# Optimization experiments

Measured on AMD Instinct MI355X. Metric: run time of the kernel, lower is better.

Reference implementation:

```python
import jax, jax.numpy as jnp
import numpy as np

NUM_HEADS = 16
THETA = 10000.0


def _rope(x, pos, theta):
    # x: [B, H, S, D], pos: [S] ints. Interleaved-pair RoPE.
    D = x.shape[-1]
    half = D // 2
    inv_freq = theta ** (-(jnp.arange(half, dtype=jnp.float32) * 2.0) / D)  # [half]
    ang = pos.astype(jnp.float32)[:, None] * inv_freq[None, :]              # [S, half]
    cos, sin = jnp.cos(ang), jnp.sin(ang)
    x1 = x[..., 0::2]
    x2 = x[..., 1::2]
    r1 = x1 * cos - x2 * sin
    r2 = x1 * sin + x2 * cos
    return jnp.stack([r1, r2], axis=-1).reshape(x.shape)


def setup_inputs() -> dict:
    key = jax.random.key(0)
    ks = jax.random.split(key, 5)
    B, S, D = 4, 2048, 1024
    scale = 1.0 / np.sqrt(D)
    x = jax.random.normal(ks[0], (B, S, D), dtype=jnp.float32)
    Wq = jax.random.normal(ks[1], (D, D), dtype=jnp.float32) * scale
    Wk = jax.random.normal(ks[2], (D, D), dtype=jnp.float32) * scale
    Wv = jax.random.normal(ks[3], (D, D), dtype=jnp.float32) * scale
    Wo = jax.random.normal(ks[4], (D, D), dtype=jnp.float32) * scale
    token_positions = jnp.arange(S, dtype=jnp.int64)
    return {"x": x, "Wq": Wq, "Wk": Wk, "Wv": Wv, "Wo": Wo,
            "token_positions": token_positions}


def reference(x, Wq, Wk, Wv, Wo, token_positions):
    B, S, D = x.shape
    H = NUM_HEADS
    hd = D // H
    # Projections (weights stored as [d_model, d_k], matching the transposed params)
    q = jnp.einsum('bsd,de->bse', x, Wq).reshape(B, S, H, hd).transpose(0, 2, 1, 3)
    k = jnp.einsum('bsd,de->bse', x, Wk).reshape(B, S, H, hd).transpose(0, 2, 1, 3)
    v = jnp.einsum('bsd,de->bse', x, Wv).reshape(B, S, H, hd).transpose(0, 2, 1, 3)
    # RoPE on q and k
    q = _rope(q, token_positions, THETA)
    k = _rope(k, token_positions, THETA)
    # Causal scaled dot-product attention
    scores = jnp.einsum('bhqd,bhkd->bhqk', q, k) / jnp.sqrt(jnp.float32(hd))
    causal = jnp.tril(jnp.ones((S, S), dtype=bool))
    scores = jnp.where(causal, scores, jnp.float32(-jnp.inf))
    attn = jax.nn.softmax(scores, axis=-1)
    o = jnp.einsum('bhqk,bhkd->bhqd', attn, v)          # [B, H, S, hd]
    o = o.transpose(0, 2, 1, 3).reshape(B, S, D)         # [B, S, D]
    return jnp.einsum('bsd,de->bse', o, Wo)
```

## Files before the change

### kernel.cpp

```cpp
#include <hip/hip_runtime.h>
#include <math.h>

#define B_ 4
#define S_ 2048
#define D_ 1024
#define H_ 16
#define HD_ 64
#define ES_F 0.180336880111f
#define KF (-0.41524101186f)

typedef unsigned short ushort_t;
typedef __attribute__((ext_vector_type(8))) short short8;
typedef __attribute__((ext_vector_type(4))) short short4_t;
typedef __attribute__((ext_vector_type(4))) float f32x4;
typedef __attribute__((ext_vector_type(16))) float f32x16;
typedef __attribute__((ext_vector_type(2))) unsigned uint2v;

typedef const void __attribute__((address_space(1))) gvoid;
typedef void __attribute__((address_space(3))) lvoid;

__device__ __forceinline__ ushort_t f2bf(float f) {
    union { float f; unsigned u; } v; v.f = f;
    unsigned r = (v.u + 0x7FFFu + ((v.u >> 16) & 1u)) >> 16;
    return (ushort_t)r;
}
__device__ __forceinline__ float fexp2(float x) {
#if __has_builtin(__builtin_amdgcn_exp2f)
    return __builtin_amdgcn_exp2f(x);
#else
    return exp2f(x);
#endif
}
__device__ __forceinline__ unsigned pk2t(float a, float b) {
    union { float f; unsigned u; } A, Bv; A.f = a; Bv.f = b;
#if __has_builtin(__builtin_amdgcn_perm)
    return __builtin_amdgcn_perm(Bv.u, A.u, 0x07060302u);
#else
    return (A.u >> 16) | (Bv.u & 0xFFFF0000u);
#endif
}
__device__ __forceinline__ short8 mk_frag(unsigned a, unsigned b, unsigned c, unsigned d) {
    union { unsigned u[4]; short8 s; } t;
    t.u[0] = a; t.u[1] = b; t.u[2] = c; t.u[3] = d; return t.s;
}

__global__ __launch_bounds__(256)
void cvt_x(const float* __restrict__ x, ushort_t* __restrict__ xb)
{
    const size_t i = ((size_t)blockIdx.x * 256 + threadIdx.x) * 8;
    float4 a = *(const float4*)&x[i];
    float4 b = *(const float4*)&x[i + 4];
    short8 o;
    o[0] = (short)f2bf(a.x); o[1] = (short)f2bf(a.y);
    o[2] = (short)f2bf(a.z); o[3] = (short)f2bf(a.w);
    o[4] = (short)f2bf(b.x); o[5] = (short)f2bf(b.y);
    o[6] = (short)f2bf(b.z); o[7] = (short)f2bf(b.w);
    *(short8*)&xb[i] = o;
}

__global__ __launch_bounds__(256)
void cvt_wt4(const float* __restrict__ W0, const float* __restrict__ W1,
             const float* __restrict__ W2, const float* __restrict__ W3,
             ushort_t* __restrict__ T0, ushort_t* __restrict__ T1,
             ushort_t* __restrict__ T2, ushort_t* __restrict__ T3)
{
    const int z = blockIdx.z;
    const float* W = (z == 0) ? W0 : (z == 1) ? W1 : (z == 2) ? W2 : W3;
    ushort_t* Wt = (z == 0) ? T0 : (z == 1) ? T1 : (z == 2) ? T2 : T3;

    __shared__ __align__(16) float T[64 * 68];
    const int t = threadIdx.x;
    const int k0 = blockIdx.y * 64, n0 = blockIdx.x * 64;
    const int row = t >> 2, c0 = (t & 3) * 16;
#pragma unroll
    for (int u = 0; u < 4; ++u)
        *(float4*)&T[row * 68 + c0 + u * 4] =
            *(const float4*)&W[(size_t)(k0 + row) * D_ + n0 + c0 + u * 4];
    __syncthreads();
    const int n = t >> 2, kc = (t & 3) * 16;
    short8 o0, o1;
#pragma unroll
    for (int kk = 0; kk < 8; ++kk) o0[kk] = (short)f2bf(T[(kc + kk) * 68 + n]);
#pragma unroll
    for (int kk = 0; kk < 8; ++kk) o1[kk] = (short)f2bf(T[(kc + 8 + kk) * 68 + n]);
    *(short8*)&Wt[(size_t)(n0 + n) * D_ + k0 + kc] = o0;
    *(short8*)&Wt[(size_t)(n0 + n) * D_ + k0 + kc + 8] = o1;
}


#define STAGE(tt, Ad, Bd) {                                                    \
    const int kk_ = (tt) * 64;                                                 \
    _Pragma("unroll") for (int i_ = 0; i_ < 4; ++i_) {                         \
        const int rb_ = (i_ * 4 + w) * 8;                                      \
        __builtin_amdgcn_global_load_lds(                                      \
            (gvoid*)&pA[(size_t)(aBase + rb_ + srow) * D_ + kk_ + sch],        \
            (lvoid*)&(Ad)[rb_ * 64], 16, 0, 0);                                \
        __builtin_amdgcn_global_load_lds(                                      \
            (gvoid*)&pB[(size_t)(bBase + rb_ + srow) * D_ + kk_ + sch],        \
            (lvoid*)&(Bd)[rb_ * 64], 16, 0, 0);                                \
    } }

#define COMPUTE(Ab, Bb) {                                                      \
    _Pragma("unroll") for (int ks = 0; ks < 4; ++ks) {                         \
        const int xr_ = (((ks * 2 + hl) ^ (lq & 7)) << 3);                     \
        short8 af0 = *(const short8*)&(Ab)[(wr * 64 + lq) * 64 + xr_];         \
        short8 af1 = *(const short8*)&(Ab)[(wr * 64 + 32 + lq) * 64 + xr_];    \
        short8 bf0 = *(const short8*)&(Bb)[(wc * 64 + lq) * 64 + xr_];         \
        short8 bf1 = *(const short8*)&(Bb)[(wc * 64 + 32 + lq) * 64 + xr_];    \
        acc[0][0] = __builtin_amdgcn_mfma_f32_32x32x16_bf16(af0, bf0, acc[0][0], 0, 0, 0); \
        acc[0][1] = __builtin_amdgcn_mfma_f32_32x32x16_bf16(af0, bf1, acc[0][1], 0, 0, 0); \
        acc[1][0] = __builtin_amdgcn_mfma_f32_32x32x16_bf16(af1, bf0, acc[1][0], 0, 0, 0); \
        acc[1][1] = __builtin_amdgcn_mfma_f32_32x32x16_bf16(af1, bf1, acc[1][1], 0, 0, 0); \
    } }

__global__ __launch_bounds__(256, 2)
void gemm_bt(const ushort_t* __restrict__ A,
             const ushort_t* __restrict__ W0, const ushort_t* __restrict__ W1,
             const ushort_t* __restrict__ W2,
             void* __restrict__ d0, void* __restrict__ d1, void* __restrict__ d2,
             const int mode_base)
{
    __shared__ __align__(16) ushort_t As[2 * 128 * 64];
    __shared__ __align__(16) ushort_t Bs[2 * 128 * 64];

    const int tid = threadIdx.x;
    const int lane = tid & 63;
    const int hl = lane >> 5;
    const int lq = lane & 31;
    const int w = tid >> 6, wr = w >> 1, wc = w & 1;
    const int z = blockIdx.z;
    const ushort_t* Wt = (z == 0) ? W0 : (z == 1) ? W1 : W2;
    const int mode = mode_base + z;
    const bool sw = (mode != 2);

    const int tokT = blockIdx.x * 128, featT = blockIdx.y * 128;
    const ushort_t* pA = sw ? Wt : A;
    const ushort_t* pB = sw ? A : Wt;
    const int aBase = sw ? featT : tokT;
    const int bBase = sw ? tokT : featT;

    const f32x16 zv16 = {0,0,0,0,0,0,0,0,0,0,0,0,0,0,0,0};
    f32x16 acc[2][2];
    acc[0][0] = zv16; acc[0][1] = zv16; acc[1][0] = zv16; acc[1][1] = zv16;

    const int srow = lane >> 3;
    const int spc  = lane & 7;
    const int sch  = (spc ^ srow) * 8;

    ushort_t* A0 = As;  ushort_t* A1 = As + 128 * 64;
    ushort_t* B0 = Bs;  ushort_t* B1 = Bs + 128 * 64;

    STAGE(0, A0, B0);
    __syncthreads();

#pragma unroll 1
    for (int t2 = 0; t2 < 8; ++t2) {
        STAGE(2 * t2 + 1, A1, B1);
        COMPUTE(A0, B0);
        __syncthreads();
        if (t2 < 7) STAGE(2 * t2 + 2, A0, B0);
        COMPUTE(A1, B1);
        __syncthreads();
    }

    if (mode == 2) {
#pragma unroll
        for (int tn = 0; tn < 2; ++tn) {
            const int n = bBase + wc * 64 + tn * 32 + lq;
            const int h = n >> 6, dd = n & 63;
#pragma unroll
            for (int tm = 0; tm < 2; ++tm) {
                const int mb = aBase + wr * 64 + tm * 32 + 4 * hl;
#pragma unroll
                for (int g = 0; g < 4; ++g) {
                    const int m_base = mb + 8 * g;
                    const int bb2 = m_base >> 11, s0 = m_base & (S_ - 1);
                    short4_t pk;
#pragma unroll
                    for (int r = 0; r < 4; ++r)
                        pk[r] = (short)f2bf(acc[tm][tn][4 * g + r]);
                    *(short4_t*)&((ushort_t*)d2)[(((size_t)bb2 * H_ + h) * HD_ + dd) * S_ + s0] = pk;
                }
            }
        }
    } else if (mode == 3) {
        float* outp = (float*)d0;
#pragma unroll
        for (int tn = 0; tn < 2; ++tn) {
            const int tok = bBase + wc * 64 + tn * 32 + lq;
#pragma unroll
            for (int tm = 0; tm < 2; ++tm) {
                const int fb = aBase + wr * 64 + tm * 32 + 4 * hl;
#pragma unroll
                for (int g = 0; g < 4; ++g) {
                    f32x4 v;
                    v[0] = acc[tm][tn][4 * g + 0];
                    v[1] = acc[tm][tn][4 * g + 1];
                    v[2] = acc[tm][tn][4 * g + 2];
                    v[3] = acc[tm][tn][4 * g + 3];
                    *(f32x4*)&outp[(size_t)tok * D_ + fb + 8 * g] = v;
                }
            }
        }
    } else {
        ushort_t* dst = (mode == 0) ? (ushort_t*)d0 : (ushort_t*)d1;
        const float sc = (mode == 0) ? ES_F : 1.0f;
#pragma unroll
        for (int tn = 0; tn < 2; ++tn) {
            const int tok = bBase + wc * 64 + tn * 32 + lq;
            const int bb2 = tok >> 11, s0 = tok & (S_ - 1);
            const float fs0 = (float)s0;
#pragma unroll
            for (int tm = 0; tm < 2; ++tm) {
                const int fb = aBase + wr * 64 + tm * 32 + 4 * hl;
                const int h = fb >> 6;
                const int ddb = fb & 63;
                ushort_t* dp = &dst[(((size_t)bb2 * H_ + h) * S_ + s0) * HD_];
#pragma unroll
                for (int g = 0; g < 4; ++g) {
                    const int dd = ddb + 8 * g;
                    const int jj = dd >> 1;
                    const float if0 = exp2f(KF * (float)jj);
                    const float if1 = exp2f(KF * (float)(jj + 1));
                    float sn0, cs0, sn1, cs1;
                    __sincosf(fs0 * if0, &sn0, &cs0);
                    __sincosf(fs0 * if1, &sn1, &cs1);
                    const float x0 = acc[tm][tn][4 * g + 0];
                    const float x1 = acc[tm][tn][4 * g + 1];
                    const float x2 = acc[tm][tn][4 * g + 2];
                    const float x3 = acc[tm][tn][4 * g + 3];
                    short4_t pk;
                    pk[0] = (short)f2bf((x0 * cs0 - x1 * sn0) * sc);
                    pk[1] = (short)f2bf((x0 * sn0 + x1 * cs0) * sc);
                    pk[2] = (short)f2bf((x2 * cs1 - x3 * sn1) * sc);
                    pk[3] = (short)f2bf((x2 * sn1 + x3 * cs1) * sc);
                    *(short4_t*)&dp[dd] = pk;
                }
            }
        }
    }
}

__global__ __launch_bounds__(256)
void attn_mfma(const ushort_t* __restrict__ Q, const ushort_t* __restrict__ K,
               const ushort_t* __restrict__ Vt, ushort_t* __restrict__ O)
{
    __shared__ __align__(16) ushort_t sK[64 * 64];
    __shared__ __align__(16) ushort_t sVt[64 * 64];

    const int tid = threadIdx.x;
    const int lane = tid & 63;
    const int hl = lane >> 5;
    const int lq = lane & 31;
    const int w = tid >> 6;
    const int hb64 = blockIdx.x;
    const int pair = blockIdx.y;
    const int h = hb64 >> 2, bb = hb64 & 3;
    const size_t hb = ((size_t)(bb * H_ + h)) * S_ * HD_;

    const int srow = lane >> 3;
    const int spc = lane & 7;

    short8 ones;
#pragma unroll
    for (int i = 0; i < 8; ++i) ones[i] = (short)0x3F80;

    const f32x16 zv16 = {0,0,0,0,0,0,0,0,0,0,0,0,0,0,0,0};

    for (int pass = 0; pass < 2; ++pass) {
        const int q0 = ((pass == 0) ? (15 - pair) : pair) * 128;
        const int wq = q0 + w * 32;
        const int qg = wq + lq;

        short8 qf[4];
#pragma unroll
        for (int ks = 0; ks < 4; ++ks)
            qf[ks] = *(const short8*)&Q[hb + (size_t)qg * HD_ + ks * 16 + hl * 8];

        f32x16 oa[2], la;
        oa[0] = zv16; oa[1] = zv16; la = zv16;

        const int nt = q0 / 64 + 2;
        for (int kt = 0; kt < nt; ++kt) {
            const int k0 = kt * 64;
            __syncthreads();
            {
#pragma unroll
                for (int i = 0; i < 2; ++i) {
                    const int row = i * 32 + w * 8 + srow;
                    const int sc = (spc ^ (row & 7)) * 8;
                    __builtin_amdgcn_global_load_lds(
                        (gvoid*)&K[hb + (size_t)(k0 + row) * HD_ + sc],
                        (lvoid*)&sK[(i * 32 + w * 8) * 64], 16, 0, 0);
                    __builtin_amdgcn_global_load_lds(
                        (gvoid*)&Vt[hb + (size_t)row * S_ + k0 + sc],
                        (lvoid*)&sVt[(i * 32 + w * 8) * 64], 16, 0, 0);
                }
            }
            __syncthreads();

            if (k0 > wq + 31) continue;

            f32x16 st[2];
            st[0] = zv16; st[1] = zv16;
            const int kr0 = lq, kr1 = 32 + lq;
#pragma unroll
            for (int ks = 0; ks < 4; ++ks) {
                const int ch = ks * 2 + hl;
                short8 ak0 = *(const short8*)&sK[kr0 * 64 + ((ch ^ (kr0 & 7)) << 3)];
                short8 ak1 = *(const short8*)&sK[kr1 * 64 + ((ch ^ (kr1 & 7)) << 3)];
                st[0] = __builtin_amdgcn_mfma_f32_32x32x16_bf16(ak0, qf[ks], st[0], 0, 0, 0);
                st[1] = __builtin_amdgcn_mfma_f32_32x32x16_bf16(ak1, qf[ks], st[1], 0, 0, 0);
            }

            const bool diag = (k0 + 63 > wq);
            short8 pf[4];
#pragma unroll
            for (int nt2 = 0; nt2 < 2; ++nt2) {
                float pv[16];
                const int kb = k0 + nt2 * 32 + 4 * hl;
#pragma unroll
                for (int g = 0; g < 4; ++g)
#pragma unroll
                    for (int r = 0; r < 4; ++r) {
                        float s = st[nt2][4 * g + r];
                        if (diag) {
                            const int key = kb + 8 * g + r;
                            s = (key <= qg) ? s : -INFINITY;
                        }
                        pv[4 * g + r] = fexp2(s);
                    }
                unsigned P2[8];
#pragma unroll
                for (int g = 0; g < 4; ++g) {
                    P2[2 * g]     = pk2t(pv[4 * g + 0], pv[4 * g + 1]);
                    P2[2 * g + 1] = pk2t(pv[4 * g + 2], pv[4 * g + 3]);
                }
#if __has_builtin(__builtin_amdgcn_permlane32_swap)
                uint2v r02 = __builtin_amdgcn_permlane32_swap(P2[0], P2[2], false, false);
                uint2v r13 = __builtin_amdgcn_permlane32_swap(P2[1], P2[3], false, false);
                uint2v r46 = __builtin_amdgcn_permlane32_swap(P2[4], P2[6], false, false);
                uint2v r57 = __builtin_amdgcn_permlane32_swap(P2[5], P2[7], false, false);
                pf[nt2 * 2 + 0] = mk_frag(r02[0], r13[0], r02[1], r13[1]);
                pf[nt2 * 2 + 1] = mk_frag(r46[0], r57[0], r46[1], r57[1]);
#else
                unsigned X[8];
#pragma unroll
                for (int m = 0; m < 8; ++m) X[m] = (unsigned)__shfl_xor((int)P2[m], 32);
                pf[nt2 * 2 + 0] = hl ? mk_frag(X[2], X[3], P2[2], P2[3])
                                     : mk_frag(P2[0], P2[1], X[0], X[1]);
                pf[nt2 * 2 + 1] = hl ? mk_frag(X[6], X[7], P2[6], P2[7])
                                     : mk_frag(P2[4], P2[5], X[4], X[5]);
#endif
            }

            const int vr0 = lq, vr1 = 32 + lq;
#pragma unroll
            for (int ks2 = 0; ks2 < 4; ++ks2) {
                const int ch = ks2 * 2 + hl;
                short8 av0 = *(const short8*)&sVt[vr0 * 64 + ((ch ^ (vr0 & 7)) << 3)];
                short8 av1 = *(const short8*)&sVt[vr1 * 64 + ((ch ^ (vr1 & 7)) << 3)];
                oa[0] = __builtin_amdgcn_mfma_f32_32x32x16_bf16(av0, pf[ks2], oa[0], 0, 0, 0);
                oa[1] = __builtin_amdgcn_mfma_f32_32x32x16_bf16(av1, pf[ks2], oa[1], 0, 0, 0);
                la    = __builtin_amdgcn_mfma_f32_32x32x16_bf16(ones, pf[ks2], la, 0, 0, 0);
            }
        }

        const float inv = 1.f / la[0];
        ushort_t* Ob = &O[((size_t)(bb * S_ + qg)) * D_ + h * HD_];
#pragma unroll
        for (int mt = 0; mt < 2; ++mt)
#pragma unroll
            for (int g = 0; g < 4; ++g) {
                short4_t pk;
#pragma unroll
                for (int r = 0; r < 4; ++r)
                    pk[r] = (short)f2bf(oa[mt][4 * g + r] * inv);
                *(short4_t*)&Ob[mt * 32 + 8 * g + 4 * hl] = pk;
            }
    }
}

extern "C" void kernel_launch(void* const* d_in, const int* in_sizes, int n_in,
                              void* d_out, int out_size, void* d_ws, size_t ws_size,
                              hipStream_t stream)
{
    (void)in_sizes; (void)n_in; (void)out_size; (void)ws_size;
    const float* x  = (const float*)d_in[0];
    const float* Wq = (const float*)d_in[1];
    const float* Wk = (const float*)d_in[2];
    const float* Wv = (const float*)d_in[3];
    const float* Wo = (const float*)d_in[4];

    float* out = (float*)d_out;
    ushort_t* ws = (ushort_t*)d_ws;
    const size_t NX = (size_t)B_ * S_ * D_;
    const size_t NW = (size_t)D_ * D_;
    ushort_t* xb  = ws;
    ushort_t* Wqt = xb + NX;
    ushort_t* Wkt = Wqt + NW;
    ushort_t* Wvt = Wkt + NW;
    ushort_t* Wot = Wvt + NW;
    ushort_t* Qb  = Wot + NW;
    ushort_t* Kb  = Qb + NX;
    ushort_t* Vtb = Kb + NX;
    ushort_t* Ob  = Vtb + NX;

    cvt_x<<<dim3(NX / 2048), 256, 0, stream>>>(x, xb);
    cvt_wt4<<<dim3(16, 16, 4), 256, 0, stream>>>(Wq, Wk, Wv, Wo, Wqt, Wkt, Wvt, Wot);

    gemm_bt<<<dim3(64, 8, 3), 256, 0, stream>>>(xb, Wqt, Wkt, Wvt, Qb, Kb, Vtb, 0);
    attn_mfma<<<dim3(64, 8), 256, 0, stream>>>(Qb, Kb, Vtb, Ob);
    gemm_bt<<<dim3(64, 8, 1), 256, 0, stream>>>(Ob, Wot, Wot, Wot, out, nullptr, nullptr, 3);
}
```

Measured before the change: 261.7 us.

## Double-buffer K/V tiles in attention and unswap output projection GEMM

The attention kernel now uses two LDS buffers for K and V tiles, issuing the next tile's async global-to-LDS loads before computing on the current tile, which halves the barriers per iteration and overlaps memory with MFMA work. MFMA sections are wrapped with s_setprio to favor matrix issue. The output projection no longer swaps operands, and its epilogue writes scalar floats with the token as row, changing the store pattern. Double LDS use may reduce occupancy.

Result: no change. 262.5 us (+0.3%).

```diff
diff --git a/kernel.cpp b/kernel.cpp
--- a/kernel.cpp
+++ b/kernel.cpp
@@ -131,7 +131,7 @@
     const int z = blockIdx.z;
     const ushort_t* Wt = (z == 0) ? W0 : (z == 1) ? W1 : W2;
     const int mode = mode_base + z;
-    const bool sw = (mode != 2);
+    const bool sw = (mode == 0) || (mode == 1);
 
     const int tokT = blockIdx.x * 128, featT = blockIdx.y * 128;
     const ushort_t* pA = sw ? Wt : A;
@@ -187,19 +187,16 @@
         float* outp = (float*)d0;
 #pragma unroll
         for (int tn = 0; tn < 2; ++tn) {
-            const int tok = bBase + wc * 64 + tn * 32 + lq;
+            const int n = bBase + wc * 64 + tn * 32 + lq;
 #pragma unroll
             for (int tm = 0; tm < 2; ++tm) {
-                const int fb = aBase + wr * 64 + tm * 32 + 4 * hl;
-#pragma unroll
-                for (int g = 0; g < 4; ++g) {
-                    f32x4 v;
-                    v[0] = acc[tm][tn][4 * g + 0];
-                    v[1] = acc[tm][tn][4 * g + 1];
-                    v[2] = acc[tm][tn][4 * g + 2];
-                    v[3] = acc[tm][tn][4 * g + 3];
-                    *(f32x4*)&outp[(size_t)tok * D_ + fb + 8 * g] = v;
-                }
+                const int mb = aBase + wr * 64 + tm * 32 + 4 * hl;
+#pragma unroll
+                for (int g = 0; g < 4; ++g)
+#pragma unroll
+                    for (int r = 0; r < 4; ++r)
+                        outp[(size_t)(mb + 8 * g + r) * D_ + n] =
+                            acc[tm][tn][4 * g + r];
             }
         }
     } else {
@@ -241,12 +238,26 @@
     }
 }
 
+
+#define ATTN_STAGE(kt_, Kd, Vd) {                                              \
+    const int k0_ = (kt_) * 64;                                                \
+    _Pragma("unroll") for (int i_ = 0; i_ < 2; ++i_) {                         \
+        const int row_ = i_ * 32 + w * 8 + srow;                               \
+        const int sc_ = (spc ^ (row_ & 7)) * 8;                                \
+        __builtin_amdgcn_global_load_lds(                                      \
+            (gvoid*)&K[hb + (size_t)(k0_ + row_) * HD_ + sc_],                 \
+            (lvoid*)&(Kd)[(i_ * 32 + w * 8) * 64], 16, 0, 0);                  \
+        __builtin_amdgcn_global_load_lds(                                      \
+            (gvoid*)&Vt[hb + (size_t)row_ * S_ + k0_ + sc_],                   \
+            (lvoid*)&(Vd)[(i_ * 32 + w * 8) * 64], 16, 0, 0);                  \
+    } }
+
 __global__ __launch_bounds__(256)
 void attn_mfma(const ushort_t* __restrict__ Q, const ushort_t* __restrict__ K,
                const ushort_t* __restrict__ Vt, ushort_t* __restrict__ O)
 {
-    __shared__ __align__(16) ushort_t sK[64 * 64];
-    __shared__ __align__(16) ushort_t sVt[64 * 64];
+    __shared__ __align__(16) ushort_t sK[2][64 * 64];
+    __shared__ __align__(16) ushort_t sVt[2][64 * 64];
 
     const int tid = threadIdx.x;
     const int lane = tid & 63;
@@ -281,89 +292,89 @@
         oa[0] = zv16; oa[1] = zv16; la = zv16;
 
         const int nt = q0 / 64 + 2;
+        ATTN_STAGE(0, sK[0], sVt[0]);
+        __syncthreads();
+
+#pragma unroll 1
         for (int kt = 0; kt < nt; ++kt) {
             const int k0 = kt * 64;
+            const int p = kt & 1;
+            if (kt + 1 < nt) ATTN_STAGE(kt + 1, sK[p ^ 1], sVt[p ^ 1]);
+
+            if (k0 <= wq + 31) {
+                const ushort_t* cK = sK[p];
+                const ushort_t* cV = sVt[p];
+
+                f32x16 st[2];
+                st[0] = zv16; st[1] = zv16;
+                const int kr0 = lq, kr1 = 32 + lq;
+                __builtin_amdgcn_s_setprio(1);
+#pragma unroll
+                for (int ks = 0; ks < 4; ++ks) {
+                    const int ch = ks * 2 + hl;
+                    short8 ak0 = *(const short8*)&cK[kr0 * 64 + ((ch ^ (kr0 & 7)) << 3)];
+                    short8 ak1 = *(const short8*)&cK[kr1 * 64 + ((ch ^ (kr1 & 7)) << 3)];
+                    st[0] = __builtin_amdgcn_mfma_f32_32x32x16_bf16(ak0, qf[ks], st[0], 0, 0, 0);
+                    st[1] = __builtin_amdgcn_mfma_f32_32x32x16_bf16(ak1, qf[ks], st[1], 0, 0, 0);
+                }
+                __builtin_amdgcn_s_setprio(0);
+
+                const bool diag = (k0 + 63 > wq);
+                short8 pf[4];
+#pragma unroll
+                for (int nt2 = 0; nt2 < 2; ++nt2) {
+                    float pv[16];
+                    const int kb = k0 + nt2 * 32 + 4 * hl;
+#pragma unroll
+                    for (int g = 0; g < 4; ++g)
+#pragma unroll
+                        for (int r = 0; r < 4; ++r) {
+                            float s = st[nt2][4 * g + r];
+                            if (diag) {
+                                const int key = kb + 8 * g + r;
+                                s = (key <= qg) ? s : -INFINITY;
+                            }
+                            pv[4 * g + r] = fexp2(s);
+                        }
+                    unsigned P2[8];
+#pragma unroll
+                    for (int g = 0; g < 4; ++g) {
+                        P2[2 * g]     = pk2t(pv[4 * g + 0], pv[4 * g + 1]);
+                        P2[2 * g + 1] = pk2t(pv[4 * g + 2], pv[4 * g + 3]);
+                    }
+#if __has_builtin(__builtin_amdgcn_permlane32_swap)
+                    uint2v r02 = __builtin_amdgcn_permlane32_swap(P2[0], P2[2], false, false);
+                    uint2v r13 = __builtin_amdgcn_permlane32_swap(P2[1], P2[3], false, false);
+                    uint2v r46 = __builtin_amdgcn_permlane32_swap(P2[4], P2[6], false, false);
+                    uint2v r57 = __builtin_amdgcn_permlane32_swap(P2[5], P2[7], false, false);
+                    pf[nt2 * 2 + 0] = mk_frag(r02[0], r13[0], r02[1], r13[1]);
+                    pf[nt2 * 2 + 1] = mk_frag(r46[0], r57[0], r46[1], r57[1]);
+#else
+                    unsigned X[8];
+#pragma unroll
+                    for (int m = 0; m < 8; ++m) X[m] = (unsigned)__shfl_xor((int)P2[m], 32);
+                    pf[nt2 * 2 + 0] = hl ? mk_frag(X[2], X[3], P2[2], P2[3])
+                                         : mk_frag(P2[0], P2[1], X[0], X[1]);
+                    pf[nt2 * 2 + 1] = hl ? mk_frag(X[6], X[7], P2[6], P2[7])
+                                         : mk_frag(P2[4], P2[5], X[4], X[5]);
+#endif
+                }
+
+                const int vr0 = lq, vr1 = 32 + lq;
+                __builtin_amdgcn_s_setprio(1);
+#pragma unroll
+                for (int ks2 = 0; ks2 < 4; ++ks2) {
+                    const int ch = ks2 * 2 + hl;
+                    short8 av0 = *(const short8*)&cV[vr0 * 64 + ((ch ^ (vr0 & 7)) << 3)];
+                    short8 av1 = *(const short8*)&cV[vr1 * 64 + ((ch ^ (vr1 & 7)) << 3)];
+                    oa[0] = __builtin_amdgcn_mfma_f32_32x32x16_bf16(av0, pf[ks2], oa[0], 0, 0, 0);
+                    oa[1] = __builtin_amdgcn_mfma_f32_32x32x16_bf16(av1, pf[ks2], oa[1], 0, 0, 0);
+                    la    = __builtin_amdgcn_mfma_f32_32x32x16_bf16(ones, pf[ks2], la, 0, 0, 0);
+                }
+                __builtin_amdgcn_s_setprio(0);
+            }
+
             __syncthreads();
-            {
-#pragma unroll
-                for (int i = 0; i < 2; ++i) {
-                    const int row = i * 32 + w * 8 + srow;
-                    const int sc = (spc ^ (row & 7)) * 8;
-                    __builtin_amdgcn_global_load_lds(
-                        (gvoid*)&K[hb + (size_t)(k0 + row) * HD_ + sc],
-                        (lvoid*)&sK[(i * 32 + w * 8) * 64], 16, 0, 0);
-                    __builtin_amdgcn_global_load_lds(
-                        (gvoid*)&Vt[hb + (size_t)row * S_ + k0 + sc],
-                        (lvoid*)&sVt[(i * 32 + w * 8) * 64], 16, 0, 0);
-                }
-            }
-            __syncthreads();
-
-            if (k0 > wq + 31) continue;
-
-            f32x16 st[2];
-            st[0] = zv16; st[1] = zv16;
-            const int kr0 = lq, kr1 = 32 + lq;
-#pragma unroll
-            for (int ks = 0; ks < 4; ++ks) {
-                const int ch = ks * 2 + hl;
-                short8 ak0 = *(const short8*)&sK[kr0 * 64 + ((ch ^ (kr0 & 7)) << 3)];
-                short8 ak1 = *(const short8*)&sK[kr1 * 64 + ((ch ^ (kr1 & 7)) << 3)];
-                st[0] = __builtin_amdgcn_mfma_f32_32x32x16_bf16(ak0, qf[ks], st[0], 0, 0, 0);
-                st[1] = __builtin_amdgcn_mfma_f32_32x32x16_bf16(ak1, qf[ks], st[1], 0, 0, 0);
-            }
-
-            const bool diag = (k0 + 63 > wq);
-            short8 pf[4];
-#pragma unroll
-            for (int nt2 = 0; nt2 < 2; ++nt2) {
-                float pv[16];
-                const int kb = k0 + nt2 * 32 + 4 * hl;
-#pragma unroll
-                for (int g = 0; g < 4; ++g)
-#pragma unroll
-                    for (int r = 0; r < 4; ++r) {
-                        float s = st[nt2][4 * g + r];
-                        if (diag) {
-                            const int key = kb + 8 * g + r;
-                            s = (key <= qg) ? s : -INFINITY;
-                        }
-                        pv[4 * g + r] = fexp2(s);
-                    }
-                unsigned P2[8];
-#pragma unroll
-                for (int g = 0; g < 4; ++g) {
-                    P2[2 * g]     = pk2t(pv[4 * g + 0], pv[4 * g + 1]);
-                    P2[2 * g + 1] = pk2t(pv[4 * g + 2], pv[4 * g + 3]);
-                }
-#if __has_builtin(__builtin_amdgcn_permlane32_swap)
-                uint2v r02 = __builtin_amdgcn_permlane32_swap(P2[0], P2[2], false, false);
-                uint2v r13 = __builtin_amdgcn_permlane32_swap(P2[1], P2[3], false, false);
-                uint2v r46 = __builtin_amdgcn_permlane32_swap(P2[4], P2[6], false, false);
-                uint2v r57 = __builtin_amdgcn_permlane32_swap(P2[5], P2[7], false, false);
-                pf[nt2 * 2 + 0] = mk_frag(r02[0], r13[0], r02[1], r13[1]);
-                pf[nt2 * 2 + 1] = mk_frag(r46[0], r57[0], r46[1], r57[1]);
-#else
-                unsigned X[8];
-#pragma unroll
-                for (int m = 0; m < 8; ++m) X[m] = (unsigned)__shfl_xor((int)P2[m], 32);
-                pf[nt2 * 2 + 0] = hl ? mk_frag(X[2], X[3], P2[2], P2[3])
-                                     : mk_frag(P2[0], P2[1], X[0], X[1]);
-                pf[nt2 * 2 + 1] = hl ? mk_frag(X[6], X[7], P2[6], P2[7])
-                                     : mk_frag(P2[4], P2[5], X[4], X[5]);
-#endif
-            }
-
-            const int vr0 = lq, vr1 = 32 + lq;
-#pragma unroll
-            for (int ks2 = 0; ks2 < 4; ++ks2) {
-                const int ch = ks2 * 2 + hl;
-                short8 av0 = *(const short8*)&sVt[vr0 * 64 + ((ch ^ (vr0 & 7)) << 3)];
-                short8 av1 = *(const short8*)&sVt[vr1 * 64 + ((ch ^ (vr1 & 7)) << 3)];
-                oa[0] = __builtin_amdgcn_mfma_f32_32x32x16_bf16(av0, pf[ks2], oa[0], 0, 0, 0);
-                oa[1] = __builtin_amdgcn_mfma_f32_32x32x16_bf16(av1, pf[ks2], oa[1], 0, 0, 0);
-                la    = __builtin_amdgcn_mfma_f32_32x32x16_bf16(ones, pf[ks2], la, 0, 0, 0);
-            }
         }
 
         const float inv = 1.f / la[0];
```
